# Optimization experiments

Measured on AMD Instinct MI355X. Metric: run time of the kernel, lower is better.

## Reference

```python
import jax, jax.numpy as jnp
import numpy as np

KERNEL = 3          # conv kernel size (stride 1)
NUM_SEG = 512       # static cap on number of pooled segments (pad semantics)
NEG = -10.0         # fill value for positions not covered by the strided conv


def _sinusoidal_pe(S, D):
    pos = np.arange(S)[:, None].astype(np.float32)
    div = np.exp(-np.log(10000.0) * (np.arange(0, D, 2).astype(np.float32) / D))
    pe = np.zeros((S, D), dtype=np.float32)
    pe[:, 0::2] = np.sin(pos * div)
    pe[:, 1::2] = np.cos(pos * div)
    return jnp.asarray(pe)


def setup_inputs() -> dict:
    key = jax.random.key(0)
    B, L, D = 8, 2048, 1024
    Ch = D // KERNEL  # 341
    ks = jax.random.split(key, 4)
    hidden = jax.random.normal(ks[0], (B, L, D), jnp.float32)
    lengths = jax.random.randint(ks[1], (B,), L // 2, L + 1)
    attention_mask = (jnp.arange(L)[None, :] < lengths[:, None]).astype(jnp.float32)
    w1 = jax.random.normal(ks[2], (Ch, D, KERNEL), jnp.float32) / np.sqrt(D * KERNEL)
    b1 = jnp.zeros((Ch,), jnp.float32)
    w2 = jax.random.normal(ks[3], (1, Ch, 1), jnp.float32) / np.sqrt(Ch)
    b2 = jnp.full((1,), -2.5, jnp.float32)  # init_for_12 bias
    return {"hidden": hidden, "attention_mask": attention_mask,
            "w1": w1, "b1": b1, "w2": w2, "b2": b2}


def reference(hidden, attention_mask, w1, b1, w2, b2):
    B, L, D = hidden.shape
    dt = hidden.dtype
    # --- strided-conv boundary logits (eval path, no Gumbel noise) ---
    x = jnp.swapaxes(hidden, 1, 2)  # (B, D, L)
    h = jax.lax.conv_general_dilated(x, w1, (1,), 'VALID',
                                     dimension_numbers=('NCH', 'OIH', 'NCH'))
    h = jax.nn.relu(h + b1[None, :, None])            # (B, Ch, L-2)
    strided = jnp.einsum('bcl,oc->bl', h, w2[:, :, 0]) + b2[0]  # (B, L-2)
    # scatter strided logits to positions kernel-1 + i (i.e. [2:L])
    logits = jnp.full((B, L), NEG, dt).at[:, KERNEL - 1:].set(strided)
    probs = jax.nn.sigmoid(logits)
    soft = probs
    hard_samp = (probs > 0.5).astype(dt)
    hard = hard_samp + soft - jax.lax.stop_gradient(soft)  # straight-through
    # --- mask and force a boundary at the last real token ---
    hard = hard * attention_mask
    pad = attention_mask == 0
    first_pad = pad & (jnp.cumsum(pad.astype(jnp.int32), axis=1) == 1)
    last_real = jnp.roll(first_pad, -1, axis=1).at[:, -1].set(False).astype(dt)
    hard = jnp.maximum(hard, last_real)
    # --- dynamic downsample: mean-pool tokens within boundary segments ---
    seg = jnp.cumsum(hard, axis=1) - hard  # segment id per token (B, L)
    sid = jnp.arange(NUM_SEG, dtype=dt)
    foo = 1.0 - jnp.clip(jnp.abs(sid[None, None, :] - seg[:, :, None]), 0.0, 1.0)  # (B,L,S)
    foo = foo * attention_mask[:, :, None]
    lel = foo / (jnp.sum(foo, axis=1, keepdims=True) + 1e-9)
    pooled = jnp.einsum('bls,bld->bsd', lel, hidden)  # (B, S, D)
    pooled = pooled + _sinusoidal_pe(NUM_SEG, D)[None].astype(dt)
    # --- shortened attention mask (stream compaction of kept positions) ---
    keep = jax.lax.stop_gradient(hard) > 0.5
    order = jnp.argsort(jnp.logical_not(keep).astype(jnp.int32), axis=1)  # stable: kept first
    gathered = jnp.take_along_axis(attention_mask, order, axis=1)[:, :NUM_SEG]
    n_keep = jnp.sum(keep, axis=1)
    valid = jnp.arange(NUM_SEG)[None, :] < n_keep[:, None]
    short_mask = jnp.where(valid, gathered, 0.0)
    num_boundaries = jnp.sum(hard)
    total_positions = jnp.sum(attention_mask)
    return pooled, num_boundaries, total_positions, short_mask
```

## Files before the change

kernel.cpp:

```cpp
#include <hip/hip_runtime.h>
#include <hip/hip_bf16.h>
#include <cmath>

#define B_SZ 8
#define L_SZ 2048
#define D_SZ 1024
#define CH 341
#define CP 384
#define LCONV 2046
#define NSEG 512
#define KDIM 3072
#define KSTEPS 48

#define POOLED_N (B_SZ * NSEG * D_SZ)

typedef _Float16 f16x8 __attribute__((ext_vector_type(8)));
typedef float f32x4 __attribute__((ext_vector_type(4)));

__device__ __forceinline__ void gl_lds16(const void* g, void* l) {
    __builtin_amdgcn_global_load_lds(
        (const __attribute__((address_space(1))) unsigned int*)g,
        (__attribute__((address_space(3))) unsigned int*)l, 16, 0, 0);
}

__global__ __launch_bounds__(256) void convert_hidden_kernel(
        const float* __restrict__ hidden, _Float16* __restrict__ hid16) {
    size_t idx = (size_t)blockIdx.x * 256 + threadIdx.x;
    float4 v0 = ((const float4*)hidden)[idx * 2];
    float4 v1 = ((const float4*)hidden)[idx * 2 + 1];
    f16x8 o;
    o[0] = (_Float16)v0.x; o[1] = (_Float16)v0.y;
    o[2] = (_Float16)v0.z; o[3] = (_Float16)v0.w;
    o[4] = (_Float16)v1.x; o[5] = (_Float16)v1.y;
    o[6] = (_Float16)v1.z; o[7] = (_Float16)v1.w;
    ((f16x8*)hid16)[idx] = o;
}

__global__ __launch_bounds__(256) void convert_w1_kernel(
        const float* __restrict__ w1, const float* __restrict__ b2,
        _Float16* __restrict__ bfrag, float* __restrict__ logits) {
    int idx = blockIdx.x * 256 + threadIdx.x;
    int j = idx & 7;
    int lane = (idx >> 3) & 63;
    int kc = (idx >> 9) & 1;
    int rest = idx >> 10;
    int s = rest % KSTEPS;
    int tt = rest / KSTEPS;
    int c = tt * 16 + (lane & 15);
    int k = s * 64 + kc * 32 + ((lane >> 4) << 3) + j;
    int kk = k >> 10, d = k & 1023;
    float v = (c < CH) ? w1[((size_t)c * 1024 + d) * 3 + kk] : 0.0f;
    bfrag[idx] = (_Float16)v;
    if (idx < B_SZ * LCONV) logits[idx] = b2[0];
}

#define LDS_BUF 8192

#define WAITV8() asm volatile("s_waitcnt vmcnt(8)" ::: "memory")
#define WAITV0() asm volatile("s_waitcnt vmcnt(0)" ::: "memory")
#define BAR()    __builtin_amdgcn_s_barrier()

#define LOAD_B(DST) do {                                                    \
    _Pragma("unroll")                                                       \
    for (int jj = 0; jj < 3; ++jj) {                                        \
        DST[jj][0] = bptr[jj][0];                                           \
        DST[jj][1] = bptr[jj][64];                                          \
        bptr[jj] += 128;                                                    \
    } } while (0)

#define ISSUE_A(OFF) do {                                                   \
    gl_lds16(pa0, lds + (OFF) + (wave * 64) * 16);                          \
    gl_lds16(pa1, lds + (OFF) + (256 + wave * 64) * 16);                    \
    pa0 += 64; pa1 += 64; } while (0)

#define COMPUTE(OFF, BSET) do {                                             \
    _Pragma("unroll")                                                       \
    for (int kc = 0; kc < 2; ++kc) {                                        \
        f16x8 a[4];                                                         \
        _Pragma("unroll")                                                   \
        for (int ii = 0; ii < 4; ++ii)                                      \
            a[ii] = *(const f16x8*)(lds + (OFF) + (kc * 256 + ii * 64 + lane) * 16); \
        _Pragma("unroll")                                                   \
        for (int ii = 0; ii < 4; ++ii)                                      \
            _Pragma("unroll")                                               \
            for (int jj = 0; jj < 3; ++jj)                                  \
                acc[ii][jj] = __builtin_amdgcn_mfma_f32_16x16x32_f16(       \
                    a[ii], BSET[jj][kc], acc[ii][jj], 0, 0, 0);             \
    } } while (0)

__global__ __launch_bounds__(256, 2) void conv_mfma_kernel(
        const _Float16* __restrict__ hid16, const _Float16* __restrict__ bfrag,
        const float* __restrict__ b1, const float* __restrict__ w2,
        float* __restrict__ logits) {
    const int nt = blockIdx.x;
    const int mt = blockIdx.y;
    const int b  = blockIdx.z;
    const int l0 = mt * 64;
    const int n0 = nt * 192;
    const int tid = threadIdx.x;
    const int wave = tid >> 6, lane = tid & 63;
    const int wn = wave;
    const int quad = lane >> 4, l16 = lane & 15;

    __shared__ __align__(16) char lds[3 * LDS_BUF];

    const _Float16* hb = hid16 + (size_t)b * L_SZ * D_SZ;

    const _Float16* pa0;
    const _Float16* pa1;
    {
        int f0 = tid;
        int m0 = ((f0 >> 6) << 4) + (f0 & 15);
        int k0 = ((f0 >> 4) & 3) * 8;
        int l = l0 + m0; if (l > LCONV - 1) l = LCONV - 1;
        pa0 = hb + (size_t)l * 1024 + k0;
        int f1 = tid;
        int m1 = ((f1 >> 6) << 4) + (f1 & 15);
        int k1 = ((f1 >> 4) & 3) * 8;
        l = l0 + m1; if (l > LCONV - 1) l = LCONV - 1;
        pa1 = hb + (size_t)l * 1024 + 32 + k1;
    }

    const f16x8* bp = (const f16x8*)bfrag;
    const f16x8* bptr[3];
    #pragma unroll
    for (int jj = 0; jj < 3; ++jj) {
        int tt = nt * 12 + wn * 3 + jj;
        bptr[jj] = bp + (size_t)tt * (KSTEPS * 2 * 64) + lane;
    }

    f32x4 acc[4][3] = {};
    f16x8 B0[3][2], B1[3][2], B2[3][2];

    LOAD_B(B0); ISSUE_A(0);
    LOAD_B(B1); ISSUE_A(LDS_BUF);

    for (int t = 0; t < 15; ++t) {
        WAITV8(); BAR();
        LOAD_B(B2); ISSUE_A(2 * LDS_BUF);
        COMPUTE(0, B0);

        WAITV8(); BAR();
        LOAD_B(B0); ISSUE_A(0);
        COMPUTE(LDS_BUF, B1);

        WAITV8(); BAR();
        LOAD_B(B1); ISSUE_A(LDS_BUF);
        COMPUTE(2 * LDS_BUF, B2);
    }
    WAITV8(); BAR();
    LOAD_B(B2); ISSUE_A(2 * LDS_BUF);
    COMPUTE(0, B0);
    WAITV8(); BAR();
    COMPUTE(LDS_BUF, B1);
    WAITV0(); BAR();
    COMPUTE(2 * LDS_BUF, B2);

    __syncthreads();

    float cb1[3], cw2[3];
    #pragma unroll
    for (int jj = 0; jj < 3; ++jj) {
        int ch = n0 + wn * 48 + jj * 16 + l16;
        bool v = ch < CH;
        cb1[jj] = v ? b1[ch] : 0.0f;
        cw2[jj] = v ? w2[ch] : 0.0f;
    }
    float* red = (float*)lds;
    #pragma unroll
    for (int ii = 0; ii < 4; ++ii)
        #pragma unroll
        for (int r = 0; r < 4; ++r) {
            float P = 0.0f;
            #pragma unroll
            for (int jj = 0; jj < 3; ++jj) {
                float h = acc[ii][jj][r] + cb1[jj];
                if (h > 0.0f) P += h * cw2[jj];
            }
            P += __shfl_xor(P, 1);
            P += __shfl_xor(P, 2);
            P += __shfl_xor(P, 4);
            P += __shfl_xor(P, 8);
            if (l16 == 0)
                red[(ii * 16 + quad * 4 + r) * 4 + wn] = P;
        }
    __syncthreads();
    if (tid < 64) {
        int l = l0 + tid;
        if (l < LCONV)
            atomicAdd(&logits[b * LCONV + l],
                      red[tid * 4] + red[tid * 4 + 1] + red[tid * 4 + 2] + red[tid * 4 + 3]);
    }
}

__global__ __launch_bounds__(256) void fixup_kernel(
        const float* __restrict__ hidden, const float* __restrict__ w1,
        const float* __restrict__ b1, const float* __restrict__ w2,
        const float* __restrict__ b2, float* __restrict__ logits) {
    const int b = blockIdx.y, l0 = blockIdx.x * 64, tid = threadIdx.x;
    __shared__ float hrow[3 * 1024];
    __shared__ float sred[256];
    __shared__ int flags[64];
    __shared__ int nflag;
    if (tid == 0) nflag = 0;
    __syncthreads();
    if (tid < 64) {
        int l = l0 + tid;
        if (l < LCONV) {
            float v = logits[b * LCONV + l];
            if (fabsf(v) < 0.02f) { int k = atomicAdd(&nflag, 1); flags[k] = l; }
        }
    }
    __syncthreads();
    const int nf = nflag;
    for (int fi = 0; fi < nf; ++fi) {
        const int l = flags[fi];
        for (int t = tid; t < 3072; t += 256)
            hrow[t] = hidden[((size_t)b * L_SZ + l) * 1024 + t];
        __syncthreads();
        float tot = 0.0f;
        for (int c = tid; c < CH; c += 256) {
            const float* wr = w1 + (size_t)c * 3072;
            float dot = 0.0f;
            for (int d = 0; d < 1024; ++d)
                dot += hrow[d] * wr[d * 3] + hrow[1024 + d] * wr[d * 3 + 1]
                     + hrow[2048 + d] * wr[d * 3 + 2];
            float h = dot + b1[c];
            if (h > 0.0f) tot += h * w2[c];
        }
        sred[tid] = tot; __syncthreads();
        for (int off = 128; off > 0; off >>= 1) {
            if (tid < off) sred[tid] += sred[tid + off];
            __syncthreads();
        }
        if (tid == 0) logits[b * LCONV + l] = sred[0] + b2[0];
        __syncthreads();
    }
}

__global__ void boundary_scan_kernel(const float* __restrict__ logits,
                                     const float* __restrict__ amask,
                                     int* __restrict__ segstart,
                                     int* __restrict__ segid,
                                     float* __restrict__ out_nb,
                                     float* __restrict__ out_tp,
                                     float* __restrict__ short_mask) {
    const int b = blockIdx.x, tid = threadIdx.x;
    __shared__ int sdata[256];
    __shared__ int s_len, s_total;

    int cnt = 0;
    #pragma unroll
    for (int j = 0; j < 8; ++j) {
        int l = tid * 8 + j;
        cnt += (amask[b * L_SZ + l] > 0.5f) ? 1 : 0;
    }
    sdata[tid] = cnt; __syncthreads();
    for (int off = 128; off > 0; off >>= 1) {
        if (tid < off) sdata[tid] += sdata[tid + off];
        __syncthreads();
    }
    if (tid == 0) s_len = sdata[0];
    __syncthreads();
    const int len = s_len;

    int bits[8]; int tsum = 0;
    #pragma unroll
    for (int j = 0; j < 8; ++j) {
        int l = tid * 8 + j;
        int h = 0;
        if (l >= 2 && l < len) h = (logits[b * LCONV + (l - 2)] > 0.0f) ? 1 : 0;
        if (len < L_SZ && l == len - 1) h = 1;
        bits[j] = h; tsum += h;
    }
    __syncthreads();
    sdata[tid] = tsum; __syncthreads();
    for (int off = 1; off < 256; off <<= 1) {
        int v = (tid >= off) ? sdata[tid - off] : 0;
        __syncthreads();
        sdata[tid] += v;
        __syncthreads();
    }
    const int texcl = sdata[tid] - tsum;
    if (tid == 255) s_total = sdata[255];
    __syncthreads();
    const int total = s_total;

    for (int s = tid; s <= NSEG; s += 256)
        segstart[b * (NSEG + 1) + s] = (s == 0) ? 0 : len;
    __syncthreads();
    int run = texcl;
    #pragma unroll
    for (int j = 0; j < 8; ++j) {
        int l = tid * 8 + j;
        int sv = -1;
        if (l < len && run < NSEG) sv = run;
        segid[b * L_SZ + l] = sv;
        if (bits[j]) {
            if (run + 1 <= NSEG) segstart[b * (NSEG + 1) + run + 1] = l + 1;
            run++;
        }
    }

    if (tid == 0) {
        atomicAdd(out_nb, (float)total);
        atomicAdd(out_tp, (float)len);
    }
    for (int s = tid; s < NSEG; s += 256)
        short_mask[b * NSEG + s] = (s < total) ? 1.0f : 0.0f;
}

__global__ __launch_bounds__(256) void pool_accum_kernel(
        const float* __restrict__ hidden, const int* __restrict__ segid,
        float* __restrict__ pooled) {
    const int chunk = blockIdx.x, b = blockIdx.y;
    const int tid = threadIdx.x;
    const int d0 = tid * 4;
    const int lbase = chunk * 16;
    const float* hb = hidden + (size_t)b * L_SZ * D_SZ + d0;
    const int* sg = segid + b * L_SZ + lbase;
    float4 acc = make_float4(0.f, 0.f, 0.f, 0.f);
    int cur = -1;
    #pragma unroll
    for (int t = 0; t < 16; ++t) {
        int sid = sg[t];
        if (sid != cur) {
            if (cur >= 0) {
                float* dst = pooled + ((size_t)(b * NSEG + cur)) * D_SZ + d0;
                atomicAdd(dst + 0, acc.x); atomicAdd(dst + 1, acc.y);
                atomicAdd(dst + 2, acc.z); atomicAdd(dst + 3, acc.w);
            }
            acc = make_float4(0.f, 0.f, 0.f, 0.f);
            cur = sid;
        }
        if (sid >= 0) {
            float4 v = *(const float4*)(hb + (size_t)(lbase + t) * D_SZ);
            acc.x += v.x; acc.y += v.y; acc.z += v.z; acc.w += v.w;
        }
    }
    if (cur >= 0) {
        float* dst = pooled + ((size_t)(b * NSEG + cur)) * D_SZ + d0;
        atomicAdd(dst + 0, acc.x); atomicAdd(dst + 1, acc.y);
        atomicAdd(dst + 2, acc.z); atomicAdd(dst + 3, acc.w);
    }
}

__global__ __launch_bounds__(256) void pool_final_kernel(
        float* __restrict__ pooled, const int* __restrict__ segstart) {
    const int s = blockIdx.x, b = blockIdx.y, tid = threadIdx.x;
    const int l0 = segstart[b * (NSEG + 1) + s];
    const int l1 = segstart[b * (NSEG + 1) + s + 1];
    const float inv = 1.0f / ((float)(l1 - l0) + 1e-9f);
    const int d0 = tid * 4;
    size_t o = ((size_t)(b * NSEG + s)) * D_SZ + d0;
    float4 v = *(float4*)(pooled + o);
    const float ce = -9.210340371976184f / 512.0f;
    const int i = d0 >> 1;
    const float a0 = (float)s * expf(ce * (float)i);
    const float a1 = (float)s * expf(ce * (float)(i + 1));
    float4 out;
    out.x = v.x * inv + sinf(a0);
    out.y = v.y * inv + cosf(a0);
    out.z = v.z * inv + sinf(a1);
    out.w = v.w * inv + cosf(a1);
    *(float4*)(pooled + o) = out;
}

extern "C" void kernel_launch(void* const* d_in, const int* in_sizes, int n_in,
                              void* d_out, int out_size, void* d_ws, size_t ws_size,
                              hipStream_t stream) {
    const float* hidden = (const float*)d_in[0];
    const float* amask  = (const float*)d_in[1];
    const float* w1     = (const float*)d_in[2];
    const float* b1     = (const float*)d_in[3];
    const float* w2     = (const float*)d_in[4];
    const float* b2     = (const float*)d_in[5];

    float* out    = (float*)d_out;
    float* pooled = out;
    float* nb     = out + POOLED_N;
    float* tp     = nb + 1;
    float* smask  = out + POOLED_N + 2;

    hipMemsetAsync(d_out, 0, (size_t)(POOLED_N + 2) * sizeof(float), stream);

    const size_t HID_E = (size_t)B_SZ * L_SZ * D_SZ;
    const size_t OFF_HID16    = 0;
    const size_t OFF_BPACK    = OFF_HID16 + HID_E * 2;
    const size_t OFF_LOGITS   = OFF_BPACK + (size_t)CP * KDIM * 2;
    const size_t OFF_SEGSTART = OFF_LOGITS + (size_t)B_SZ * LCONV * 4;
    const size_t OFF_SEGID    = OFF_SEGSTART + (size_t)B_SZ * (NSEG + 1) * 4;

    _Float16* hid16  = (_Float16*)((char*)d_ws + OFF_HID16);
    _Float16* bfrag  = (_Float16*)((char*)d_ws + OFF_BPACK);
    float*    logits = (float*)((char*)d_ws + OFF_LOGITS);
    int*      segst  = (int*)((char*)d_ws + OFF_SEGSTART);
    int*      segid  = (int*)((char*)d_ws + OFF_SEGID);

    convert_hidden_kernel<<<(int)(HID_E / 8 / 256), 256, 0, stream>>>(hidden, hid16);
    convert_w1_kernel<<<(CP * KDIM) / 256, 256, 0, stream>>>(w1, b2, bfrag, logits);
    conv_mfma_kernel<<<dim3(2, 32, B_SZ), 256, 0, stream>>>(hid16, bfrag, b1, w2, logits);
    fixup_kernel<<<dim3(32, B_SZ), 256, 0, stream>>>(hidden, w1, b1, w2, b2, logits);
    boundary_scan_kernel<<<B_SZ, 256, 0, stream>>>(logits, amask, segst, segid, nb, tp, smask);
    pool_accum_kernel<<<dim3(128, B_SZ), 256, 0, stream>>>(hidden, segid, pooled);
    pool_final_kernel<<<dim3(NSEG, B_SZ), 256, 0, stream>>>(pooled, segst);
}
```

Before: 232.8 us.

## Pool segments by direct per-segment gather instead of atomic scatter

Replaces the atomic-scatter pooling kernel plus finalize kernel with a single kernel where each block owns one segment and sums hidden rows between segstart bounds, then applies the mean and positional encoding. This removes the segid array, per-element float atomics, and the full memset of the pooled output (only the two scalars are zeroed). The cost is load imbalance: segment lengths vary, and long final segments (up to the padding length) are handled serially by one block.

Measured after the change: 728.6 us. 3.13x slower.

```diff
diff --git a/kernel.cpp b/kernel.cpp
--- a/kernel.cpp
+++ b/kernel.cpp
@@ -241,7 +241,6 @@
 __global__ void boundary_scan_kernel(const float* __restrict__ logits,
                                      const float* __restrict__ amask,
                                      int* __restrict__ segstart,
-                                     int* __restrict__ segid,
                                      float* __restrict__ out_nb,
                                      float* __restrict__ out_tp,
                                      float* __restrict__ short_mask) {
@@ -293,9 +292,6 @@
     #pragma unroll
     for (int j = 0; j < 8; ++j) {
         int l = tid * 8 + j;
-        int sv = -1;
-        if (l < len && run < NSEG) sv = run;
-        segid[b * L_SZ + l] = sv;
         if (bits[j]) {
             if (run + 1 <= NSEG) segstart[b * (NSEG + 1) + run + 1] = l + 1;
             run++;
@@ -310,60 +306,30 @@
         short_mask[b * NSEG + s] = (s < total) ? 1.0f : 0.0f;
 }
 
-__global__ __launch_bounds__(256) void pool_accum_kernel(
-        const float* __restrict__ hidden, const int* __restrict__ segid,
+__global__ __launch_bounds__(256) void pool_kernel(
+        const float* __restrict__ hidden, const int* __restrict__ segstart,
         float* __restrict__ pooled) {
-    const int chunk = blockIdx.x, b = blockIdx.y;
-    const int tid = threadIdx.x;
-    const int d0 = tid * 4;
-    const int lbase = chunk * 16;
-    const float* hb = hidden + (size_t)b * L_SZ * D_SZ + d0;
-    const int* sg = segid + b * L_SZ + lbase;
-    float4 acc = make_float4(0.f, 0.f, 0.f, 0.f);
-    int cur = -1;
-    #pragma unroll
-    for (int t = 0; t < 16; ++t) {
-        int sid = sg[t];
-        if (sid != cur) {
-            if (cur >= 0) {
-                float* dst = pooled + ((size_t)(b * NSEG + cur)) * D_SZ + d0;
-                atomicAdd(dst + 0, acc.x); atomicAdd(dst + 1, acc.y);
-                atomicAdd(dst + 2, acc.z); atomicAdd(dst + 3, acc.w);
-            }
-            acc = make_float4(0.f, 0.f, 0.f, 0.f);
-            cur = sid;
-        }
-        if (sid >= 0) {
-            float4 v = *(const float4*)(hb + (size_t)(lbase + t) * D_SZ);
-            acc.x += v.x; acc.y += v.y; acc.z += v.z; acc.w += v.w;
-        }
-    }
-    if (cur >= 0) {
-        float* dst = pooled + ((size_t)(b * NSEG + cur)) * D_SZ + d0;
-        atomicAdd(dst + 0, acc.x); atomicAdd(dst + 1, acc.y);
-        atomicAdd(dst + 2, acc.z); atomicAdd(dst + 3, acc.w);
-    }
-}
-
-__global__ __launch_bounds__(256) void pool_final_kernel(
-        float* __restrict__ pooled, const int* __restrict__ segstart) {
     const int s = blockIdx.x, b = blockIdx.y, tid = threadIdx.x;
     const int l0 = segstart[b * (NSEG + 1) + s];
     const int l1 = segstart[b * (NSEG + 1) + s + 1];
+    const int d0 = tid * 4;
+    const float* hb = hidden + (size_t)b * L_SZ * D_SZ + d0;
+    float4 acc = make_float4(0.f, 0.f, 0.f, 0.f);
+    for (int l = l0; l < l1; ++l) {
+        float4 v = *(const float4*)(hb + (size_t)l * D_SZ);
+        acc.x += v.x; acc.y += v.y; acc.z += v.z; acc.w += v.w;
+    }
     const float inv = 1.0f / ((float)(l1 - l0) + 1e-9f);
-    const int d0 = tid * 4;
-    size_t o = ((size_t)(b * NSEG + s)) * D_SZ + d0;
-    float4 v = *(float4*)(pooled + o);
     const float ce = -9.210340371976184f / 512.0f;
     const int i = d0 >> 1;
     const float a0 = (float)s * expf(ce * (float)i);
     const float a1 = (float)s * expf(ce * (float)(i + 1));
     float4 out;
-    out.x = v.x * inv + sinf(a0);
-    out.y = v.y * inv + cosf(a0);
-    out.z = v.z * inv + sinf(a1);
-    out.w = v.w * inv + cosf(a1);
-    *(float4*)(pooled + o) = out;
+    out.x = acc.x * inv + sinf(a0);
+    out.y = acc.y * inv + cosf(a0);
+    out.z = acc.z * inv + sinf(a1);
+    out.w = acc.w * inv + cosf(a1);
+    *(float4*)(pooled + ((size_t)(b * NSEG + s)) * D_SZ + d0) = out;
 }
 
 extern "C" void kernel_launch(void* const* d_in, const int* in_sizes, int n_in,
@@ -382,26 +348,23 @@
     float* tp     = nb + 1;
     float* smask  = out + POOLED_N + 2;
 
-    hipMemsetAsync(d_out, 0, (size_t)(POOLED_N + 2) * sizeof(float), stream);
+    hipMemsetAsync(nb, 0, 2 * sizeof(float), stream);
 
     const size_t HID_E = (size_t)B_SZ * L_SZ * D_SZ;
     const size_t OFF_HID16    = 0;
     const size_t OFF_BPACK    = OFF_HID16 + HID_E * 2;
     const size_t OFF_LOGITS   = OFF_BPACK + (size_t)CP * KDIM * 2;
     const size_t OFF_SEGSTART = OFF_LOGITS + (size_t)B_SZ * LCONV * 4;
-    const size_t OFF_SEGID    = OFF_SEGSTART + (size_t)B_SZ * (NSEG + 1) * 4;
 
     _Float16* hid16  = (_Float16*)((char*)d_ws + OFF_HID16);
     _Float16* bfrag  = (_Float16*)((char*)d_ws + OFF_BPACK);
     float*    logits = (float*)((char*)d_ws + OFF_LOGITS);
     int*      segst  = (int*)((char*)d_ws + OFF_SEGSTART);
-    int*      segid  = (int*)((char*)d_ws + OFF_SEGID);
 
     convert_hidden_kernel<<<(int)(HID_E / 8 / 256), 256, 0, stream>>>(hidden, hid16);
     convert_w1_kernel<<<(CP * KDIM) / 256, 256, 0, stream>>>(w1, b2, bfrag, logits);
     conv_mfma_kernel<<<dim3(2, 32, B_SZ), 256, 0, stream>>>(hid16, bfrag, b1, w2, logits);
     fixup_kernel<<<dim3(32, B_SZ), 256, 0, stream>>>(hidden, w1, b1, w2, b2, logits);
-    boundary_scan_kernel<<<B_SZ, 256, 0, stream>>>(logits, amask, segst, segid, nb, tp, smask);
-    pool_accum_kernel<<<dim3(128, B_SZ), 256, 0, stream>>>(hidden, segid, pooled);
-    pool_final_kernel<<<dim3(NSEG, B_SZ), 256, 0, stream>>>(pooled, segst);
-}
+    boundary_scan_kernel<<<B_SZ, 256, 0, stream>>>(logits, amask, segst, nb, tp, smask);
+    pool_kernel<<<dim3(NSEG, B_SZ), 256, 0, stream>>>(hidden, segst, pooled);
+}
```
